# Optimization experiments

Measured on AMD Instinct MI355X. Metric: run time of the kernel, lower is better.

Reference implementation:

```python
import jax, jax.numpy as jnp
import numpy as np

N_NODES = 50000
N_EDGES = 800000
IN_C, HID_C, OUT_C = 128, 128, 64


def setup_inputs() -> dict:
    key = jax.random.key(0)
    k1, k2, k3, k4 = jax.random.split(key, 4)
    x = jax.random.normal(k1, (N_NODES, IN_C), dtype=jnp.float32)
    edge_index = jax.random.randint(k2, (2, N_EDGES), 0, N_NODES, dtype=jnp.int64)
    # Glorot-ish init for weights, zero bias (PyG GCNConv default has bias)
    W1 = jax.random.normal(k3, (IN_C, HID_C), dtype=jnp.float32) * (1.0 / np.sqrt(IN_C))
    b1 = jnp.zeros((HID_C,), dtype=jnp.float32)
    W2 = jax.random.normal(k4, (HID_C, OUT_C), dtype=jnp.float32) * (1.0 / np.sqrt(HID_C))
    b2 = jnp.zeros((OUT_C,), dtype=jnp.float32)
    return {"x": x, "edge_index": edge_index, "W1": W1, "b1": b1, "W2": W2, "b2": b2}


def _gcn_norm(edge_index, num_nodes):
    """PyG gcn_norm: add self-loops, symmetric deg^{-1/2} normalization."""
    loop = jnp.arange(num_nodes, dtype=edge_index.dtype)
    src = jnp.concatenate([edge_index[0], loop])  # [E + N]
    dst = jnp.concatenate([edge_index[1], loop])
    ones = jnp.ones(src.shape[0], dtype=jnp.float32)
    deg = jax.ops.segment_sum(ones, dst, num_segments=num_nodes)  # in-degree incl. self-loop
    dinv = jnp.where(deg > 0, jax.lax.rsqrt(deg), 0.0)
    norm = dinv[src] * dinv[dst]  # [E + N]
    return src, dst, norm


def _gcn_conv(x, W, b, src, dst, norm, num_nodes):
    h = x @ W                                   # [N, C_out] transform first (PyG order)
    msg = h[src] * norm[:, None]                # gather + normalize, [E+N, C_out]
    out = jax.ops.segment_sum(msg, dst, num_segments=num_nodes)  # scatter-add
    return out + b


def reference(x, edge_index, W1, b1, W2, b2):
    N = x.shape[0]
    src, dst, norm = _gcn_norm(edge_index, N)  # graph normalization shared by both layers
    h = jax.nn.relu(_gcn_conv(x, W1, b1, src, dst, norm, N))
    out = _gcn_conv(h, W2, b2, src, dst, norm, N)
    return out
```

## Files before the change

### kernel.cpp

```cpp
#include <hip/hip_runtime.h>
#include <hip/hip_bf16.h>

#define IN_C  128
#define HID_C 128
#define OUT_CC 64
#define BK    128
#define CAPLG 12

using short8  = __attribute__((ext_vector_type(8))) short;
using float4v = __attribute__((ext_vector_type(4))) float;

__device__ __forceinline__ unsigned short f2b(float f) {
    unsigned int u = __float_as_uint(f);
    return (unsigned short)((u + 0x7fffu + ((u >> 16) & 1u)) >> 16);
}
__device__ __forceinline__ unsigned int pack2(float a, float b) {
    return (unsigned int)f2b(a) | ((unsigned int)f2b(b) << 16);
}
__device__ __forceinline__ float2 bf2_to_f2(unsigned int v) {
    float2 r;
    r.x = __uint_as_float(v << 16);
    r.y = __uint_as_float(v & 0xffff0000u);
    return r;
}


__global__ __launch_bounds__(256) void k_bpart(const int* __restrict__ ei,
                                               int* __restrict__ bfill,
                                               int* __restrict__ ebuf, int E, int NBK,
                                               int NCHK,
                                               const float* __restrict__ W1,
                                               const float* __restrict__ W2,
                                               unsigned short* __restrict__ w1f,
                                               unsigned short* __restrict__ w2f) {
    const int t = threadIdx.x;
    if ((int)blockIdx.x >= NCHK) {
        int e = ((int)blockIdx.x - NCHK) * 256 + t;
        if (e < 16384) {
            int j = e & 7, lane = (e >> 3) & 63, ks = (e >> 9) & 3, nt = e >> 11;
            int k = ks * 32 + ((lane >> 4) << 3) + j;
            int n = nt * 16 + (lane & 15);
            w1f[e] = f2b(W1[k * 128 + n]);
        } else if (e < 16384 + 8192) {
            int e2 = e - 16384;
            int j = e2 & 7, lane = (e2 >> 3) & 63, ks = (e2 >> 9) & 3, nt = e2 >> 11;
            int k = ks * 32 + ((lane >> 4) << 3) + j;
            int n = nt * 16 + (lane & 15);
            w2f[e2] = f2b(W2[k * 64 + n]);
        }
        return;
    }
    __shared__ int lh[512];
    __shared__ int lbase[512];
    __shared__ int s_st;
    for (int i = t; i < NBK; i += 256) lh[i] = 0;
    if (t < 64) {
        int ev = ei[2 * t], od = ei[2 * t + 1];
        unsigned long long onz = __ballot(od != 0);
        unsigned long long enz = __ballot(ev != 0);
        if (t == 0) s_st = (onz == 0ull && enz != 0ull) ? 2 : 1;
    }
    __syncthreads();
    const int st = s_st;
    const int base = blockIdx.x * 2048;
    int s[8], d[8];
    #pragma unroll
    for (int j = 0; j < 8; ++j) {
        int i = base + j * 256 + t;
        if (i < E) {
            s[j] = ei[(size_t)st * i];
            d[j] = ei[(size_t)st * ((size_t)E + i)];
            atomicAdd(&lh[d[j] >> 7], 1);
        } else d[j] = -1;
    }
    __syncthreads();
    for (int i = t; i < NBK; i += 256) {
        int c = lh[i];
        lbase[i] = c ? atomicAdd(&bfill[i], c) : 0;
        lh[i] = 0;
    }
    __syncthreads();
    #pragma unroll
    for (int j = 0; j < 8; ++j) {
        if (d[j] >= 0) {
            int b = d[j] >> 7;
            int r = lbase[b] + atomicAdd(&lh[b], 1);
            if (r < (1 << CAPLG))
                ebuf[(b << CAPLG) + r] = s[j] | ((d[j] & (BK - 1)) << 20);
        }
    }
}

__global__ __launch_bounds__(256) void k_blmg1(const int* __restrict__ ebuf,
                                               const int* __restrict__ bfill,
                                               int2* __restrict__ begend,
                                               float* __restrict__ dinv,
                                               int* __restrict__ col,
                                               const float* __restrict__ x,
                                               const unsigned short* __restrict__ w1f,
                                               unsigned short* __restrict__ h,
                                               int N, int NBK) {
    __shared__ unsigned short lds[64 * 136];
    __shared__ int cnt64[64];
    const int t = threadIdx.x;

    if ((int)blockIdx.x < NBK) {
        int* cnt = (int*)lds;
        int* sc  = cnt + BK;
        int* off = sc + BK;
        const int n0 = blockIdx.x * BK;
        const int beg = (int)blockIdx.x << CAPLG;
        const int ecnt = min(bfill[blockIdx.x], 1 << CAPLG);
        if (t < BK) cnt[t] = 0;
        __syncthreads();
        for (int i = t; i < ecnt; i += 256)
            atomicAdd(&cnt[ebuf[beg + i] >> 20], 1);
        __syncthreads();
        if (t < BK) sc[t] = cnt[t];
        __syncthreads();
        for (int o = 1; o < BK; o <<= 1) {
            int v = (t < BK && t >= o) ? sc[t - o] : 0;
            __syncthreads();
            if (t < BK) sc[t] += v;
            __syncthreads();
        }
        if (t < BK) {
            int c = cnt[t];
            off[t] = sc[t] - c;
            if (n0 + t < N) {
                begend[n0 + t] = make_int2(beg + off[t], beg + sc[t]);
                dinv[n0 + t] = rsqrtf((float)c + 1.0f);
            }
            cnt[t] = 0;
        }
        __syncthreads();
        for (int i = t; i < ecnt; i += 256) {
            int e = ebuf[beg + i];
            int dl = e >> 20;
            int p = beg + off[dl] + atomicAdd(&cnt[dl], 1);
            col[p] = e & 0xFFFFF;
        }
        return;
    }

    const int tile = (int)blockIdx.x - NBK;
    const int row0 = tile * 64;
    const int bkt  = row0 >> 7;
    const int half = (row0 >> 6) & 1;
    if (t < 64) cnt64[t] = 0;
    __syncthreads();
    {
        const int ebeg = bkt << CAPLG;
        const int ecnt = min(bfill[bkt], 1 << CAPLG);
        for (int i = t; i < ecnt; i += 256) {
            int dl = ebuf[ebeg + i] >> 20;
            if ((dl >> 6) == half) atomicAdd(&cnt64[dl & 63], 1);
        }
    }
    {
        int r = t >> 2, cc = (t & 3) * 32;
        int grow = row0 + r;
        unsigned int* dst = (unsigned int*)&lds[r * 136 + cc];
        if (grow < N) {
            const float4* src = (const float4*)(x + (size_t)grow * 128 + cc);
            #pragma unroll
            for (int i = 0; i < 8; ++i) {
                float4 v = src[i];
                dst[2 * i]     = pack2(v.x, v.y);
                dst[2 * i + 1] = pack2(v.z, v.w);
            }
        } else {
            #pragma unroll
            for (int i = 0; i < 16; ++i) dst[i] = 0;
        }
    }
    __syncthreads();
    const int w = t >> 6, lane = t & 63;
    const int quad = lane >> 4, m = lane & 15;
    short8 a[4];
    #pragma unroll
    for (int ks = 0; ks < 4; ++ks)
        a[ks] = *(const short8*)&lds[(w * 16 + m) * 136 + ks * 32 + quad * 8];
    float4v acc[8];
    #pragma unroll
    for (int nt = 0; nt < 8; ++nt) acc[nt] = (float4v){0.f, 0.f, 0.f, 0.f};
    const short8* wf = (const short8*)w1f;
    #pragma unroll
    for (int nt = 0; nt < 8; ++nt)
        #pragma unroll
        for (int ks = 0; ks < 4; ++ks)
            acc[nt] = __builtin_amdgcn_mfma_f32_16x16x32_bf16(a[ks], wf[(nt * 4 + ks) * 64 + lane],
                                                              acc[nt], 0, 0, 0);
    float drr[4];
    #pragma unroll
    for (int r = 0; r < 4; ++r) {
        int lr = w * 16 + quad * 4 + r;
        drr[r] = rsqrtf((float)cnt64[lr] + 1.0f);
    }
    #pragma unroll
    for (int nt = 0; nt < 8; ++nt)
        #pragma unroll
        for (int r = 0; r < 4; ++r) {
            int grow = row0 + w * 16 + quad * 4 + r;
            if (grow < N) h[(size_t)grow * 128 + nt * 16 + m] = f2b(acc[nt][r] * drr[r]);
        }
}

#define ACC16(u) { float2 q; \
    q = bf2_to_f2(u.x); a0 += q.x; a1 += q.y; \
    q = bf2_to_f2(u.y); a2 += q.x; a3 += q.y; \
    q = bf2_to_f2(u.z); a4 += q.x; a5 += q.y; \
    q = bf2_to_f2(u.w); a6 += q.x; a7 += q.y; }

#define PIPE_GATHER8(FEATP, ROWSTRIDE, LANEOFF) \
    int c0, c1, c2, c3, c4, c5, c6, c7; \
    if (e + 8 <= end) { \
        c0 = col[e];     c1 = col[e + 1]; c2 = col[e + 2]; c3 = col[e + 3]; \
        c4 = col[e + 4]; c5 = col[e + 5]; c6 = col[e + 6]; c7 = col[e + 7]; \
    } \
    for (; e + 16 <= end; e += 8) { \
        uint4 u0 = FEATP[(size_t)c0 * ROWSTRIDE + LANEOFF]; \
        uint4 u1 = FEATP[(size_t)c1 * ROWSTRIDE + LANEOFF]; \
        uint4 u2 = FEATP[(size_t)c2 * ROWSTRIDE + LANEOFF]; \
        uint4 u3 = FEATP[(size_t)c3 * ROWSTRIDE + LANEOFF]; \
        uint4 u4 = FEATP[(size_t)c4 * ROWSTRIDE + LANEOFF]; \
        uint4 u5 = FEATP[(size_t)c5 * ROWSTRIDE + LANEOFF]; \
        uint4 u6 = FEATP[(size_t)c6 * ROWSTRIDE + LANEOFF]; \
        uint4 u7 = FEATP[(size_t)c7 * ROWSTRIDE + LANEOFF]; \
        c0 = col[e + 8];  c1 = col[e + 9];  c2 = col[e + 10]; c3 = col[e + 11]; \
        c4 = col[e + 12]; c5 = col[e + 13]; c6 = col[e + 14]; c7 = col[e + 15]; \
        ACC16(u0) ACC16(u1) ACC16(u2) ACC16(u3) \
        ACC16(u4) ACC16(u5) ACC16(u6) ACC16(u7) \
    } \
    if (e + 8 <= end) { \
        uint4 u0 = FEATP[(size_t)c0 * ROWSTRIDE + LANEOFF]; \
        uint4 u1 = FEATP[(size_t)c1 * ROWSTRIDE + LANEOFF]; \
        uint4 u2 = FEATP[(size_t)c2 * ROWSTRIDE + LANEOFF]; \
        uint4 u3 = FEATP[(size_t)c3 * ROWSTRIDE + LANEOFF]; \
        uint4 u4 = FEATP[(size_t)c4 * ROWSTRIDE + LANEOFF]; \
        uint4 u5 = FEATP[(size_t)c5 * ROWSTRIDE + LANEOFF]; \
        uint4 u6 = FEATP[(size_t)c6 * ROWSTRIDE + LANEOFF]; \
        uint4 u7 = FEATP[(size_t)c7 * ROWSTRIDE + LANEOFF]; \
        ACC16(u0) ACC16(u1) ACC16(u2) ACC16(u3) \
        ACC16(u4) ACC16(u5) ACC16(u6) ACC16(u7) \
        e += 8; \
    } \
    if (e + 4 <= end) { \
        int d0 = col[e], d1 = col[e + 1], d2 = col[e + 2], d3 = col[e + 3]; \
        uint4 u0 = FEATP[(size_t)d0 * ROWSTRIDE + LANEOFF]; \
        uint4 u1 = FEATP[(size_t)d1 * ROWSTRIDE + LANEOFF]; \
        uint4 u2 = FEATP[(size_t)d2 * ROWSTRIDE + LANEOFF]; \
        uint4 u3 = FEATP[(size_t)d3 * ROWSTRIDE + LANEOFF]; \
        ACC16(u0) ACC16(u1) ACC16(u2) ACC16(u3) \
        e += 4; \
    } \
    for (; e < end; ++e) { \
        uint4 u = FEATP[(size_t)col[e] * ROWSTRIDE + LANEOFF]; \
        ACC16(u) \
    }

__global__ __launch_bounds__(256) void k_aggmg2(const uint4* __restrict__ feat,
                                                const int2* __restrict__ begend,
                                                const int* __restrict__ col,
                                                const float* __restrict__ dinv,
                                                const float* __restrict__ b1,
                                                const unsigned short* __restrict__ w2f,
                                                unsigned short* __restrict__ h2, int N) {
    __shared__ unsigned short lds[16 * 136];
    __shared__ float dvs[16];
    const int grp = threadIdx.x >> 4;
    const int l16 = threadIdx.x & 15;
    const int node = blockIdx.x * 16 + grp;
    float a0 = 0.f, a1 = 0.f, a2 = 0.f, a3 = 0.f, a4 = 0.f, a5 = 0.f, a6 = 0.f, a7 = 0.f;
    if (node < N) {
        const float dd = dinv[node];
        if (l16 == 0) dvs[grp] = dd;
        const int2 be = begend[node];
        int e = be.x; const int end = be.y;
        {
            uint4 sv = feat[(size_t)node * 16 + l16];
            float2 q;
            q = bf2_to_f2(sv.x); a0 = q.x; a1 = q.y;
            q = bf2_to_f2(sv.y); a2 = q.x; a3 = q.y;
            q = bf2_to_f2(sv.z); a4 = q.x; a5 = q.y;
            q = bf2_to_f2(sv.w); a6 = q.x; a7 = q.y;
        }
        PIPE_GATHER8(feat, 16, l16)
        float4 ba = ((const float4*)b1)[2 * l16];
        float4 bb = ((const float4*)b1)[2 * l16 + 1];
        a0 = fmaxf(a0 * dd + ba.x, 0.0f);
        a1 = fmaxf(a1 * dd + ba.y, 0.0f);
        a2 = fmaxf(a2 * dd + ba.z, 0.0f);
        a3 = fmaxf(a3 * dd + ba.w, 0.0f);
        a4 = fmaxf(a4 * dd + bb.x, 0.0f);
        a5 = fmaxf(a5 * dd + bb.y, 0.0f);
        a6 = fmaxf(a6 * dd + bb.z, 0.0f);
        a7 = fmaxf(a7 * dd + bb.w, 0.0f);
    } else if (l16 == 0) dvs[grp] = 0.f;
    {
        uint4 o;
        o.x = pack2(a0, a1);
        o.y = pack2(a2, a3);
        o.z = pack2(a4, a5);
        o.w = pack2(a6, a7);
        *(uint4*)&lds[grp * 136 + l16 * 8] = o;
    }
    __syncthreads();
    const int w = threadIdx.x >> 6, lane = threadIdx.x & 63;
    const int quad = lane >> 4, m = lane & 15;
    short8 a[4];
    #pragma unroll
    for (int ks = 0; ks < 4; ++ks)
        a[ks] = *(const short8*)&lds[m * 136 + ks * 32 + quad * 8];
    float4v acc = (float4v){0.f, 0.f, 0.f, 0.f};
    const short8* wf = (const short8*)w2f;
    #pragma unroll
    for (int ks = 0; ks < 4; ++ks)
        acc = __builtin_amdgcn_mfma_f32_16x16x32_bf16(a[ks], wf[(w * 4 + ks) * 64 + lane],
                                                      acc, 0, 0, 0);
    const int node0 = blockIdx.x * 16;
    #pragma unroll
    for (int r = 0; r < 4; ++r) {
        int gn = node0 + quad * 4 + r;
        if (gn < N) h2[(size_t)gn * 64 + w * 16 + m] = f2b(acc[r] * dvs[quad * 4 + r]);
    }
}

__global__ __launch_bounds__(256) void k_agg64(const uint4* __restrict__ feat,
                                               const int2* __restrict__ begend,
                                               const int* __restrict__ col,
                                               const float* __restrict__ dinv,
                                               const float* __restrict__ bias,
                                               float* __restrict__ out, int N) {
    const int grp = threadIdx.x >> 3;
    const int l8  = threadIdx.x & 7;
    const int node = blockIdx.x * 32 + grp;
    if (node >= N) return;
    const float dd = dinv[node];
    const int2 be = begend[node];
    int e = be.x; const int end = be.y;
    float a0, a1, a2, a3, a4, a5, a6, a7;
    {
        uint4 sv = feat[(size_t)node * 8 + l8];
        float2 q;
        q = bf2_to_f2(sv.x); a0 = q.x; a1 = q.y;
        q = bf2_to_f2(sv.y); a2 = q.x; a3 = q.y;
        q = bf2_to_f2(sv.z); a4 = q.x; a5 = q.y;
        q = bf2_to_f2(sv.w); a6 = q.x; a7 = q.y;
    }
    PIPE_GATHER8(feat, 8, l8)
    float4 ba = ((const float4*)bias)[2 * l8];
    float4 bb = ((const float4*)bias)[2 * l8 + 1];
    float4 o1, o2;
    o1.x = a0 * dd + ba.x;
    o1.y = a1 * dd + ba.y;
    o1.z = a2 * dd + ba.z;
    o1.w = a3 * dd + ba.w;
    o2.x = a4 * dd + bb.x;
    o2.y = a5 * dd + bb.y;
    o2.z = a6 * dd + bb.z;
    o2.w = a7 * dd + bb.w;
    float4* op = (float4*)out + (size_t)node * 16 + 2 * l8;
    op[0] = o1;
    op[1] = o2;
}

extern "C" void kernel_launch(void* const* d_in, const int* in_sizes, int n_in,
                              void* d_out, int out_size, void* d_ws, size_t ws_size,
                              hipStream_t stream) {
    const float* x  = (const float*)d_in[0];
    const int*   ei = (const int*)d_in[1];
    const float* W1 = (const float*)d_in[2];
    const float* b1 = (const float*)d_in[3];
    const float* W2 = (const float*)d_in[4];
    const float* b2 = (const float*)d_in[5];

    const int N = in_sizes[0] / IN_C;
    const int E = in_sizes[1] / 2;
    const int NBK  = (N + BK - 1) / BK;
    const int NCHK = (E + 2047) / 2048;
    const int NT1  = (N + 63) / 64;

    char* ws = (char*)d_ws;
    int*            bfill   = (int*)(ws + 64);
    int2*           begend  = (int2*)(ws + 4096);
    float*          dinv    = (float*)(ws + 404480);
    unsigned short* w1f     = (unsigned short*)(ws + 604672);
    unsigned short* w2f     = (unsigned short*)(ws + 637440);
    int*            ebuf    = (int*)(ws + 655360);
    int*            col     = (int*)(ws + 7061504);
    unsigned short* h       = (unsigned short*)(ws + 13467904);
    unsigned short* h2      = (unsigned short*)(ws + 26267904);

    hipMemsetAsync(bfill, 0, NBK * sizeof(int), stream);

    k_bpart<<<NCHK + 96, 256, 0, stream>>>(ei, bfill, ebuf, E, NBK, NCHK,
                                           W1, W2, w1f, w2f);

    k_blmg1<<<NBK + NT1, 256, 0, stream>>>(ebuf, bfill, begend, dinv, col,
                                           x, w1f, h, N, NBK);

    k_aggmg2<<<(N + 15) / 16, 256, 0, stream>>>((const uint4*)h, begend, col, dinv, b1,
                                                w2f, h2, N);

    k_agg64<<<(N + 31) / 32, 256, 0, stream>>>((const uint4*)h2, begend, col, dinv, b2,
                                               (float*)d_out, N);
}
```

Measured before the change: 168.8 us.

## Split each node's edge gather across two lane groups and reduce with shuffles

Both aggregation kernels now give each node two lane groups, each handling alternating edges (stride 2), and combine the partial sums with a cross-lane xor shuffle. k_aggmg2 moves to 512-thread blocks, with only the first 256 threads running the MFMA stage, and k_agg64 now handles 16 nodes per block instead of 32. The goal is more memory-level parallelism and shorter per-node dependency chains on the average degree of about 17. In exchange, the unroll depth per group is halved, there is extra shuffle work, and the second half of the threads sits idle during the MFMA and store phases.

New measurement: 164.3 us. 1.03x faster.

```diff
diff --git a/kernel.cpp b/kernel.cpp
--- a/kernel.cpp
+++ b/kernel.cpp
@@ -212,54 +212,33 @@
     q = bf2_to_f2(u.z); a4 += q.x; a5 += q.y; \
     q = bf2_to_f2(u.w); a6 += q.x; a7 += q.y; }
 
-#define PIPE_GATHER8(FEATP, ROWSTRIDE, LANEOFF) \
-    int c0, c1, c2, c3, c4, c5, c6, c7; \
-    if (e + 8 <= end) { \
-        c0 = col[e];     c1 = col[e + 1]; c2 = col[e + 2]; c3 = col[e + 3]; \
-        c4 = col[e + 4]; c5 = col[e + 5]; c6 = col[e + 6]; c7 = col[e + 7]; \
-    } \
-    for (; e + 16 <= end; e += 8) { \
+#define PIPE_GATHER_S2(FEATP, ROWSTRIDE, LANEOFF) \
+    int ee = e + sub; \
+    int c0, c1, c2, c3; \
+    if (ee + 6 < end) { c0 = col[ee]; c1 = col[ee + 2]; c2 = col[ee + 4]; c3 = col[ee + 6]; } \
+    for (; ee + 14 < end; ee += 8) { \
+        int p0 = col[ee + 8], p1 = col[ee + 10], p2 = col[ee + 12], p3 = col[ee + 14]; \
         uint4 u0 = FEATP[(size_t)c0 * ROWSTRIDE + LANEOFF]; \
         uint4 u1 = FEATP[(size_t)c1 * ROWSTRIDE + LANEOFF]; \
         uint4 u2 = FEATP[(size_t)c2 * ROWSTRIDE + LANEOFF]; \
         uint4 u3 = FEATP[(size_t)c3 * ROWSTRIDE + LANEOFF]; \
-        uint4 u4 = FEATP[(size_t)c4 * ROWSTRIDE + LANEOFF]; \
-        uint4 u5 = FEATP[(size_t)c5 * ROWSTRIDE + LANEOFF]; \
-        uint4 u6 = FEATP[(size_t)c6 * ROWSTRIDE + LANEOFF]; \
-        uint4 u7 = FEATP[(size_t)c7 * ROWSTRIDE + LANEOFF]; \
-        c0 = col[e + 8];  c1 = col[e + 9];  c2 = col[e + 10]; c3 = col[e + 11]; \
-        c4 = col[e + 12]; c5 = col[e + 13]; c6 = col[e + 14]; c7 = col[e + 15]; \
         ACC16(u0) ACC16(u1) ACC16(u2) ACC16(u3) \
-        ACC16(u4) ACC16(u5) ACC16(u6) ACC16(u7) \
+        c0 = p0; c1 = p1; c2 = p2; c3 = p3; \
     } \
-    if (e + 8 <= end) { \
+    if (ee + 6 < end) { \
         uint4 u0 = FEATP[(size_t)c0 * ROWSTRIDE + LANEOFF]; \
         uint4 u1 = FEATP[(size_t)c1 * ROWSTRIDE + LANEOFF]; \
         uint4 u2 = FEATP[(size_t)c2 * ROWSTRIDE + LANEOFF]; \
         uint4 u3 = FEATP[(size_t)c3 * ROWSTRIDE + LANEOFF]; \
-        uint4 u4 = FEATP[(size_t)c4 * ROWSTRIDE + LANEOFF]; \
-        uint4 u5 = FEATP[(size_t)c5 * ROWSTRIDE + LANEOFF]; \
-        uint4 u6 = FEATP[(size_t)c6 * ROWSTRIDE + LANEOFF]; \
-        uint4 u7 = FEATP[(size_t)c7 * ROWSTRIDE + LANEOFF]; \
         ACC16(u0) ACC16(u1) ACC16(u2) ACC16(u3) \
-        ACC16(u4) ACC16(u5) ACC16(u6) ACC16(u7) \
-        e += 8; \
+        ee += 8; \
     } \
-    if (e + 4 <= end) { \
-        int d0 = col[e], d1 = col[e + 1], d2 = col[e + 2], d3 = col[e + 3]; \
-        uint4 u0 = FEATP[(size_t)d0 * ROWSTRIDE + LANEOFF]; \
-        uint4 u1 = FEATP[(size_t)d1 * ROWSTRIDE + LANEOFF]; \
-        uint4 u2 = FEATP[(size_t)d2 * ROWSTRIDE + LANEOFF]; \
-        uint4 u3 = FEATP[(size_t)d3 * ROWSTRIDE + LANEOFF]; \
-        ACC16(u0) ACC16(u1) ACC16(u2) ACC16(u3) \
-        e += 4; \
-    } \
-    for (; e < end; ++e) { \
-        uint4 u = FEATP[(size_t)col[e] * ROWSTRIDE + LANEOFF]; \
+    for (; ee < end; ee += 2) { \
+        uint4 u = FEATP[(size_t)col[ee] * ROWSTRIDE + LANEOFF]; \
         ACC16(u) \
     }
 
-__global__ __launch_bounds__(256) void k_aggmg2(const uint4* __restrict__ feat,
+__global__ __launch_bounds__(512) void k_aggmg2(const uint4* __restrict__ feat,
                                                 const int2* __restrict__ begend,
                                                 const int* __restrict__ col,
                                                 const float* __restrict__ dinv,
@@ -268,24 +247,26 @@
                                                 unsigned short* __restrict__ h2, int N) {
     __shared__ unsigned short lds[16 * 136];
     __shared__ float dvs[16];
-    const int grp = threadIdx.x >> 4;
-    const int l16 = threadIdx.x & 15;
+    const int grp = threadIdx.x >> 5;
+    const int l32 = threadIdx.x & 31;
+    const int sub = l32 >> 4;
+    const int l16 = l32 & 15;
     const int node = blockIdx.x * 16 + grp;
     float a0 = 0.f, a1 = 0.f, a2 = 0.f, a3 = 0.f, a4 = 0.f, a5 = 0.f, a6 = 0.f, a7 = 0.f;
     if (node < N) {
         const float dd = dinv[node];
-        if (l16 == 0) dvs[grp] = dd;
+        if (l32 == 0) dvs[grp] = dd;
         const int2 be = begend[node];
-        int e = be.x; const int end = be.y;
-        {
+        const int e = be.x, end = be.y;
+        if (sub == 0) {
             uint4 sv = feat[(size_t)node * 16 + l16];
-            float2 q;
-            q = bf2_to_f2(sv.x); a0 = q.x; a1 = q.y;
-            q = bf2_to_f2(sv.y); a2 = q.x; a3 = q.y;
-            q = bf2_to_f2(sv.z); a4 = q.x; a5 = q.y;
-            q = bf2_to_f2(sv.w); a6 = q.x; a7 = q.y;
-        }
-        PIPE_GATHER8(feat, 16, l16)
+            ACC16(sv)
+        }
+        PIPE_GATHER_S2(feat, 16, l16)
+        a0 += __shfl_xor(a0, 16); a1 += __shfl_xor(a1, 16);
+        a2 += __shfl_xor(a2, 16); a3 += __shfl_xor(a3, 16);
+        a4 += __shfl_xor(a4, 16); a5 += __shfl_xor(a5, 16);
+        a6 += __shfl_xor(a6, 16); a7 += __shfl_xor(a7, 16);
         float4 ba = ((const float4*)b1)[2 * l16];
         float4 bb = ((const float4*)b1)[2 * l16 + 1];
         a0 = fmaxf(a0 * dd + ba.x, 0.0f);
@@ -296,8 +277,8 @@
         a5 = fmaxf(a5 * dd + bb.y, 0.0f);
         a6 = fmaxf(a6 * dd + bb.z, 0.0f);
         a7 = fmaxf(a7 * dd + bb.w, 0.0f);
-    } else if (l16 == 0) dvs[grp] = 0.f;
-    {
+    } else if (l32 == 0) dvs[grp] = 0.f;
+    if (sub == 0) {
         uint4 o;
         o.x = pack2(a0, a1);
         o.y = pack2(a2, a3);
@@ -306,23 +287,25 @@
         *(uint4*)&lds[grp * 136 + l16 * 8] = o;
     }
     __syncthreads();
-    const int w = threadIdx.x >> 6, lane = threadIdx.x & 63;
-    const int quad = lane >> 4, m = lane & 15;
-    short8 a[4];
-    #pragma unroll
-    for (int ks = 0; ks < 4; ++ks)
-        a[ks] = *(const short8*)&lds[m * 136 + ks * 32 + quad * 8];
-    float4v acc = (float4v){0.f, 0.f, 0.f, 0.f};
-    const short8* wf = (const short8*)w2f;
-    #pragma unroll
-    for (int ks = 0; ks < 4; ++ks)
-        acc = __builtin_amdgcn_mfma_f32_16x16x32_bf16(a[ks], wf[(w * 4 + ks) * 64 + lane],
-                                                      acc, 0, 0, 0);
-    const int node0 = blockIdx.x * 16;
-    #pragma unroll
-    for (int r = 0; r < 4; ++r) {
-        int gn = node0 + quad * 4 + r;
-        if (gn < N) h2[(size_t)gn * 64 + w * 16 + m] = f2b(acc[r] * dvs[quad * 4 + r]);
+    if (threadIdx.x < 256) {
+        const int w = threadIdx.x >> 6, lane = threadIdx.x & 63;
+        const int quad = lane >> 4, m = lane & 15;
+        short8 a[4];
+        #pragma unroll
+        for (int ks = 0; ks < 4; ++ks)
+            a[ks] = *(const short8*)&lds[m * 136 + ks * 32 + quad * 8];
+        float4v acc = (float4v){0.f, 0.f, 0.f, 0.f};
+        const short8* wf = (const short8*)w2f;
+        #pragma unroll
+        for (int ks = 0; ks < 4; ++ks)
+            acc = __builtin_amdgcn_mfma_f32_16x16x32_bf16(a[ks], wf[(w * 4 + ks) * 64 + lane],
+                                                          acc, 0, 0, 0);
+        const int node0 = blockIdx.x * 16;
+        #pragma unroll
+        for (int r = 0; r < 4; ++r) {
+            int gn = node0 + quad * 4 + r;
+            if (gn < N) h2[(size_t)gn * 64 + w * 16 + m] = f2b(acc[r] * dvs[quad * 4 + r]);
+        }
     }
 }
 
@@ -332,37 +315,41 @@
                                                const float* __restrict__ dinv,
                                                const float* __restrict__ bias,
                                                float* __restrict__ out, int N) {
-    const int grp = threadIdx.x >> 3;
-    const int l8  = threadIdx.x & 7;
-    const int node = blockIdx.x * 32 + grp;
+    const int grp = threadIdx.x >> 4;
+    const int l16 = threadIdx.x & 15;
+    const int sub = l16 >> 3;
+    const int l8  = l16 & 7;
+    const int node = blockIdx.x * 16 + grp;
     if (node >= N) return;
     const float dd = dinv[node];
     const int2 be = begend[node];
-    int e = be.x; const int end = be.y;
-    float a0, a1, a2, a3, a4, a5, a6, a7;
-    {
+    const int e = be.x, end = be.y;
+    float a0 = 0.f, a1 = 0.f, a2 = 0.f, a3 = 0.f, a4 = 0.f, a5 = 0.f, a6 = 0.f, a7 = 0.f;
+    if (sub == 0) {
         uint4 sv = feat[(size_t)node * 8 + l8];
-        float2 q;
-        q = bf2_to_f2(sv.x); a0 = q.x; a1 = q.y;
-        q = bf2_to_f2(sv.y); a2 = q.x; a3 = q.y;
-        q = bf2_to_f2(sv.z); a4 = q.x; a5 = q.y;
-        q = bf2_to_f2(sv.w); a6 = q.x; a7 = q.y;
-    }
-    PIPE_GATHER8(feat, 8, l8)
-    float4 ba = ((const float4*)bias)[2 * l8];
-    float4 bb = ((const float4*)bias)[2 * l8 + 1];
-    float4 o1, o2;
-    o1.x = a0 * dd + ba.x;
-    o1.y = a1 * dd + ba.y;
-    o1.z = a2 * dd + ba.z;
-    o1.w = a3 * dd + ba.w;
-    o2.x = a4 * dd + bb.x;
-    o2.y = a5 * dd + bb.y;
-    o2.z = a6 * dd + bb.z;
-    o2.w = a7 * dd + bb.w;
-    float4* op = (float4*)out + (size_t)node * 16 + 2 * l8;
-    op[0] = o1;
-    op[1] = o2;
+        ACC16(sv)
+    }
+    PIPE_GATHER_S2(feat, 8, l8)
+    a0 += __shfl_xor(a0, 8); a1 += __shfl_xor(a1, 8);
+    a2 += __shfl_xor(a2, 8); a3 += __shfl_xor(a3, 8);
+    a4 += __shfl_xor(a4, 8); a5 += __shfl_xor(a5, 8);
+    a6 += __shfl_xor(a6, 8); a7 += __shfl_xor(a7, 8);
+    if (sub == 0) {
+        float4 ba = ((const float4*)bias)[2 * l8];
+        float4 bb = ((const float4*)bias)[2 * l8 + 1];
+        float4 o1, o2;
+        o1.x = a0 * dd + ba.x;
+        o1.y = a1 * dd + ba.y;
+        o1.z = a2 * dd + ba.z;
+        o1.w = a3 * dd + ba.w;
+        o2.x = a4 * dd + bb.x;
+        o2.y = a5 * dd + bb.y;
+        o2.z = a6 * dd + bb.z;
+        o2.w = a7 * dd + bb.w;
+        float4* op = (float4*)out + (size_t)node * 16 + 2 * l8;
+        op[0] = o1;
+        op[1] = o2;
+    }
 }
 
 extern "C" void kernel_launch(void* const* d_in, const int* in_sizes, int n_in,
@@ -400,9 +387,9 @@
     k_blmg1<<<NBK + NT1, 256, 0, stream>>>(ebuf, bfill, begend, dinv, col,
                                            x, w1f, h, N, NBK);
 
-    k_aggmg2<<<(N + 15) / 16, 256, 0, stream>>>((const uint4*)h, begend, col, dinv, b1,
+    k_aggmg2<<<(N + 15) / 16, 512, 0, stream>>>((const uint4*)h, begend, col, dinv, b1,
                                                 w2f, h2, N);
 
-    k_agg64<<<(N + 31) / 32, 256, 0, stream>>>((const uint4*)h2, begend, col, dinv, b2,
+    k_agg64<<<(N + 15) / 16, 256, 0, stream>>>((const uint4*)h2, begend, col, dinv, b2,
                                                (float*)d_out, N);
 }
```
